# Optimization experiments

Hardware: AMD Instinct MI355X
Metric: run time of the kernel (lower is better)

## Reference

```python
import jax, jax.numpy as jnp
import numpy as np

N, D, H, O, E, K = 4096, 512, 1024, 512, 8, 2


def setup_inputs() -> dict:
    key = jax.random.key(0)
    ks = jax.random.split(key, 7)
    s = 0.02
    return {
        "x": jax.random.normal(ks[0], (N, D), dtype=jnp.float32),
        "W1": jax.random.normal(ks[1], (E, D, H), dtype=jnp.float32) * s,
        "b1": jnp.zeros((E, H), dtype=jnp.float32),
        "W2": jax.random.normal(ks[2], (E, H, O), dtype=jnp.float32) * s,
        "b2": jnp.zeros((E, O), dtype=jnp.float32),
        "Wg": jax.random.normal(ks[3], (D, E), dtype=jnp.float32) * s,
        "bg": jnp.zeros((E,), dtype=jnp.float32),
        "k": K,
    }


def reference(x, W1, b1, W2, b2, Wg, bg, k):
    # Gating: softmax over experts, then top-k with renormalized weights
    gates = jax.nn.softmax(x @ Wg + bg, axis=1)              # [N, E]
    topv, topi = jax.lax.top_k(gates, k)                     # [N, k]
    w = topv / jnp.sum(topv, axis=1, keepdims=True)          # renormalized top-k weights

    # Dense per-expert two-layer MLP (grouped GEMM form)
    h = jax.nn.relu(jnp.einsum('nd,edh->neh', x, W1) + b1[None])   # [N, E, H]
    y = jnp.einsum('neh,eho->neo', h, W2) + b2[None]               # [N, E, O]

    # Gather selected experts and combine
    y_sel = jnp.take_along_axis(y, topi[:, :, None], axis=1)       # [N, k, O]
    out = jnp.einsum('nko,nk->no', y_sel, w)                       # [N, O]
    return out, gates, topi
```

## Files before the change

### kernel.cpp

```cpp
#include <hip/hip_runtime.h>
#include <hip/hip_bf16.h>

#define N_TOK 4096
#define DIM   512
#define HID   1024
#define OUTD  512
#define NEXP  8
#define TOPK  2

#define MT1 72
#define HROWS 9216

typedef __bf16 bf16;
typedef bf16  bf16x8 __attribute__((ext_vector_type(8)));
typedef bf16  bf16x4 __attribute__((ext_vector_type(4)));
typedef float f32x4  __attribute__((ext_vector_type(4)));

__device__ inline f32x4 mfma16(bf16x8 a, bf16x8 b, f32x4 c) {
    return __builtin_amdgcn_mfma_f32_16x16x32_bf16(a, b, c, 0, 0, 0);
}

__device__ inline void gload16(const bf16* g, char* l) {
    __builtin_amdgcn_global_load_lds(
        (const __attribute__((address_space(1))) void*)g,
        (__attribute__((address_space(3))) void*)l, 16, 0, 0);
}

__global__ __launch_bounds__(256) void prep_gate_kernel(
    const float* __restrict__ W1, const float* __restrict__ W2,
    const float* __restrict__ Wg, const float* __restrict__ bg,
    const float* __restrict__ x,
    bf16* __restrict__ W1t, bf16* __restrict__ W2t,
    bf16* __restrict__ xb,
    float* __restrict__ gates_out, float* __restrict__ topi_out,
    int* __restrict__ pick_e, float* __restrict__ pick_w)
{
    __shared__ __align__(16) float smem[NEXP * DIM];
    int b = blockIdx.x;

    if (b >= 8192) {
        const float4* Wg4 = (const float4*)Wg;
        for (int i = threadIdx.x; i < DIM * NEXP / 4; i += 256) {
            float4 v = Wg4[i];
#pragma unroll
            for (int j = 0; j < 4; ++j) {
                int idx = i * 4 + j;
                smem[(idx & 7) * DIM + (idx >> 3)] = ((const float*)&v)[j];
            }
        }
        __syncthreads();

        int wave = threadIdx.x >> 6;
        int lane = threadIdx.x & 63;
        int n = (b - 8192) * 4 + wave;

        const float4* x4 = (const float4*)(x + (size_t)n * DIM);
        float4 v0 = x4[lane];
        float4 v1 = x4[lane + 64];

        bf16x4 o0 = { (bf16)v0.x, (bf16)v0.y, (bf16)v0.z, (bf16)v0.w };
        bf16x4 o1 = { (bf16)v1.x, (bf16)v1.y, (bf16)v1.z, (bf16)v1.w };
        bf16x4* xb4 = (bf16x4*)(xb + (size_t)n * DIM);
        xb4[lane]      = o0;
        xb4[lane + 64] = o1;

        float acc[NEXP];
#pragma unroll
        for (int e = 0; e < NEXP; ++e) {
            const float4* wr = (const float4*)(smem + e * DIM);
            float4 w0 = wr[lane];
            float4 w1 = wr[lane + 64];
            acc[e] = v0.x * w0.x + v0.y * w0.y + v0.z * w0.z + v0.w * w0.w
                   + v1.x * w1.x + v1.y * w1.y + v1.z * w1.z + v1.w * w1.w;
        }
#pragma unroll
        for (int off = 32; off >= 1; off >>= 1) {
#pragma unroll
            for (int e = 0; e < NEXP; ++e) acc[e] += __shfl_xor(acc[e], off, 64);
        }
#pragma unroll
        for (int e = 0; e < NEXP; ++e) acc[e] += bg[e];

        float m = acc[0];
#pragma unroll
        for (int e = 1; e < NEXP; ++e) m = fmaxf(m, acc[e]);
        float g[NEXP];
        float s = 0.f;
#pragma unroll
        for (int e = 0; e < NEXP; ++e) { g[e] = expf(acc[e] - m); s += g[e]; }
        float inv_s = 1.f / s;
#pragma unroll
        for (int e = 0; e < NEXP; ++e) g[e] *= inv_s;

        if (lane < NEXP) gates_out[n * NEXP + lane] = g[lane];

        if (lane == 0) {
            int m1 = 0;
#pragma unroll
            for (int e = 1; e < NEXP; ++e) if (g[e] > g[m1]) m1 = e;
            int m2 = (m1 == 0) ? 1 : 0;
#pragma unroll
            for (int e = 0; e < NEXP; ++e) if (e != m1 && g[e] > g[m2]) m2 = e;
            float v1g = g[m1], v2g = g[m2];
            float inv = 1.f / (v1g + v2g);
            topi_out[n * TOPK + 0] = (float)m1;
            topi_out[n * TOPK + 1] = (float)m2;
            int2 pe = { m1, m2 };
            float2 pw = { v1g * inv, v2g * inv };
            *(int2*)(pick_e + n * 2) = pe;
            *(float2*)(pick_w + n * 2) = pw;
        }
        return;
    }

    float (*tile)[33] = (float(*)[33])smem;
    const float* src; bf16* dst; int R, C, tilex, rem, e;
    if (b < 4096) {
        e = b >> 9; rem = b & 511; R = DIM; C = HID; tilex = 32;
        src = W1; dst = W1t;
    } else {
        b -= 4096;
        e = b >> 9; rem = b & 511; R = HID; C = OUTD; tilex = 16;
        src = W2; dst = W2t;
    }
    const float* s = src + (size_t)e * R * C;
    bf16* d = dst + (size_t)e * R * C;
    int c0 = (rem % tilex) * 32, r0 = (rem / tilex) * 32;

    int tx = threadIdx.x & 31, ty = threadIdx.x >> 5;
#pragma unroll
    for (int i = 0; i < 4; ++i) {
        int r = ty + i * 8;
        tile[r][tx] = s[(size_t)(r0 + r) * C + c0 + tx];
    }
    __syncthreads();

    int t = threadIdx.x;
    int dc = t >> 3, q = t & 7;
    bf16x4 v;
#pragma unroll
    for (int j = 0; j < 4; ++j) v[j] = (bf16)tile[q * 4 + j][dc];
    *(bf16x4*)(d + (size_t)(c0 + dc) * R + r0 + q * 4) = v;
}

__global__ __launch_bounds__(1024) void bucket_sched_kernel(
    const int* __restrict__ pick_e,
    int* __restrict__ counts, int* __restrict__ tlist, int* __restrict__ meta)
{
    __shared__ int cnt[NEXP];
    if (threadIdx.x < NEXP) cnt[threadIdx.x] = 0;
    __syncthreads();
    for (int i = threadIdx.x; i < N_TOK * 2; i += 1024) {
        int e = pick_e[i];
        int p = atomicAdd(&cnt[e], 1);
        tlist[e * N_TOK + p] = i;
    }
    __syncthreads();
    if (threadIdx.x == 0) {
        int base = 0, t1 = 0;
        for (int e = 0; e < NEXP; ++e) {
            int c = cnt[e];
            counts[e] = c;
            int n1 = (c + 127) >> 7;
            for (int lt = 0; lt < n1; ++lt) {
                meta[2 + t1 * 3]     = e;
                meta[2 + t1 * 3 + 1] = base + lt * 128;
                meta[2 + t1 * 3 + 2] = lt * 128;
                ++t1;
            }
            base += n1 << 7;
        }
        meta[0] = t1;
    }
}


__global__ __launch_bounds__(256, 4) void l1_kernel(
    const bf16* __restrict__ xb, const bf16* __restrict__ W1t,
    const float* __restrict__ b1, const int* __restrict__ counts,
    const int* __restrict__ tlist, const int* __restrict__ meta,
    bf16* __restrict__ h)
{
    int mt = blockIdx.x >> 3, nt = blockIdx.x & 7;
    if (mt >= meta[0]) return;
    const int* s1 = meta + 2 + mt * 3;
    int e = s1[0], rb = s1[1], i0 = s1[2];
    int cnt = counts[e];

    __shared__ __align__(16) char lds[32768];

    int tid = threadIdx.x, w = tid >> 6, l = tid & 63;
    int c0 = w * 128 + l, c1 = c0 + 64;
    int rA0 = c0 >> 2, rA1 = c1 >> 2;
    int kA0 = (c0 & 3) ^ ((rA0 & 3) ^ ((rA0 >> 2) & 1));
    int kA1 = (c1 & 3) ^ ((rA1 & 3) ^ ((rA1 >> 2) & 1));
    int iA0 = i0 + rA0, iA1 = i0 + rA1;
    int tok0 = iA0 < cnt ? (tlist[e * N_TOK + iA0] >> 1) : 0;
    int tok1 = iA1 < cnt ? (tlist[e * N_TOK + iA1] >> 1) : 0;
    const bf16* sA0 = xb + (size_t)tok0 * DIM + kA0 * 8;
    const bf16* sA1 = xb + (size_t)tok1 * DIM + kA1 * 8;
    int n0 = nt * 128;
    const bf16* w1e = W1t + (size_t)e * HID * DIM;
    const bf16* sB0 = w1e + (size_t)(n0 + rA0) * DIM + kA0 * 8;
    const bf16* sB1 = w1e + (size_t)(n0 + rA1) * DIM + kA1 * 8;
    int oA0 = c0 * 16, oA1 = c1 * 16;

    f32x4 acc[4][4];
#pragma unroll
    for (int mf = 0; mf < 4; ++mf)
#pragma unroll
        for (int nf = 0; nf < 4; ++nf) acc[mf][nf] = (f32x4){0.f, 0.f, 0.f, 0.f};

    int wm = w >> 1, wn = w & 1;
    int lr = l & 15;
    int kb = (((l >> 4) ^ ((l & 3) ^ ((l >> 2) & 1)))) * 16;

    {
        char* A = lds;       char* B = lds + 8192;
        gload16(sA0, A + oA0); gload16(sA1, A + oA1);
        gload16(sB0, B + oA0); gload16(sB1, B + oA1);
    }

    for (int ks = 0; ks < 16; ++ks) {
        __syncthreads();
        if (ks < 15) {
            char* A = lds + (((ks + 1) & 1) * 16384);
            char* B = A + 8192;
            int kof = (ks + 1) * 32;
            gload16(sA0 + kof, A + oA0); gload16(sA1 + kof, A + oA1);
            gload16(sB0 + kof, B + oA0); gload16(sB1 + kof, B + oA1);
        }
        char* A = lds + ((ks & 1) * 16384);
        char* B = A + 8192;
        bf16x8 af[4], bfr[4];
#pragma unroll
        for (int mf = 0; mf < 4; ++mf)
            af[mf] = *(const bf16x8*)(A + (wm * 64 + mf * 16 + lr) * 64 + kb);
#pragma unroll
        for (int nf = 0; nf < 4; ++nf)
            bfr[nf] = *(const bf16x8*)(B + (wn * 64 + nf * 16 + lr) * 64 + kb);
#pragma unroll
        for (int mf = 0; mf < 4; ++mf)
#pragma unroll
            for (int nf = 0; nf < 4; ++nf)
                acc[mf][nf] = mfma16(af[mf], bfr[nf], acc[mf][nf]);
    }

    const float* b1e = b1 + e * HID;
#pragma unroll
    for (int nf = 0; nf < 4; ++nf) {
        int colg = n0 + wn * 64 + nf * 16 + lr;
        float bias = b1e[colg];
#pragma unroll
        for (int mf = 0; mf < 4; ++mf) {
#pragma unroll
            for (int r = 0; r < 4; ++r) {
                int gr = rb + wm * 64 + mf * 16 + (l >> 4) * 4 + r;
                float v = fmaxf(acc[mf][nf][r] + bias, 0.f);
                h[(size_t)gr * HID + colg] = (bf16)v;
            }
        }
    }
}

__global__ __launch_bounds__(256, 4) void l2_kernel(
    const bf16* __restrict__ h, const bf16* __restrict__ W2t,
    const int* __restrict__ counts, const int* __restrict__ tlist,
    const int* __restrict__ meta, bf16* __restrict__ ybuf)
{
    int mt = blockIdx.x >> 2, nt = blockIdx.x & 3;
    if (mt >= meta[0]) return;
    const int* s1 = meta + 2 + mt * 3;
    int e = s1[0], rb = s1[1], i0 = s1[2];
    int cnt = counts[e];

    __shared__ __align__(16) char lds[32768];

    int tid = threadIdx.x, w = tid >> 6, l = tid & 63;
    int c0 = w * 128 + l, c1 = c0 + 64;
    int rA0 = c0 >> 2, rA1 = c1 >> 2;
    int kA0 = (c0 & 3) ^ ((rA0 & 3) ^ ((rA0 >> 2) & 1));
    int kA1 = (c1 & 3) ^ ((rA1 & 3) ^ ((rA1 >> 2) & 1));
    const bf16* sA0 = h + (size_t)(rb + rA0) * HID + kA0 * 8;
    const bf16* sA1 = h + (size_t)(rb + rA1) * HID + kA1 * 8;
    int n0 = nt * 128;
    const bf16* w2e = W2t + (size_t)e * OUTD * HID;
    const bf16* sB0 = w2e + (size_t)(n0 + rA0) * HID + kA0 * 8;
    const bf16* sB1 = w2e + (size_t)(n0 + rA1) * HID + kA1 * 8;
    int oA0 = c0 * 16, oA1 = c1 * 16;

    f32x4 acc[4][4];
#pragma unroll
    for (int mf = 0; mf < 4; ++mf)
#pragma unroll
        for (int nf = 0; nf < 4; ++nf) acc[mf][nf] = (f32x4){0.f, 0.f, 0.f, 0.f};

    int wm = w >> 1, wn = w & 1;
    int lr = l & 15;
    int kb = (((l >> 4) ^ ((l & 3) ^ ((l >> 2) & 1)))) * 16;

    {
        char* A = lds;       char* B = lds + 8192;
        gload16(sA0, A + oA0); gload16(sA1, A + oA1);
        gload16(sB0, B + oA0); gload16(sB1, B + oA1);
    }

    for (int ks = 0; ks < 32; ++ks) {
        __syncthreads();
        if (ks < 31) {
            char* A = lds + (((ks + 1) & 1) * 16384);
            char* B = A + 8192;
            int kof = (ks + 1) * 32;
            gload16(sA0 + kof, A + oA0); gload16(sA1 + kof, A + oA1);
            gload16(sB0 + kof, B + oA0); gload16(sB1 + kof, B + oA1);
        }
        char* A = lds + ((ks & 1) * 16384);
        char* B = A + 8192;
        bf16x8 af[4], bfr[4];
#pragma unroll
        for (int mf = 0; mf < 4; ++mf)
            af[mf] = *(const bf16x8*)(A + (wm * 64 + mf * 16 + lr) * 64 + kb);
#pragma unroll
        for (int nf = 0; nf < 4; ++nf)
            bfr[nf] = *(const bf16x8*)(B + (wn * 64 + nf * 16 + lr) * 64 + kb);
#pragma unroll
        for (int mf = 0; mf < 4; ++mf)
#pragma unroll
            for (int nf = 0; nf < 4; ++nf)
                acc[mf][nf] = mfma16(af[mf], bfr[nf], acc[mf][nf]);
    }

#pragma unroll
    for (int mf = 0; mf < 4; ++mf) {
#pragma unroll
        for (int r = 0; r < 4; ++r) {
            int rloc = wm * 64 + mf * 16 + (l >> 4) * 4 + r;
            int i = i0 + rloc;
            if (i < cnt) {
                int pi = tlist[e * N_TOK + i];
                bf16* yrow = ybuf + (size_t)pi * OUTD;
#pragma unroll
                for (int nf = 0; nf < 4; ++nf) {
                    int colg = n0 + wn * 64 + nf * 16 + lr;
                    yrow[colg] = (bf16)acc[mf][nf][r];
                }
            }
        }
    }
}

__global__ __launch_bounds__(256) void combine_kernel(
    const bf16* __restrict__ ybuf, const float* __restrict__ b2,
    const int* __restrict__ pick_e, const float* __restrict__ pick_w,
    float* __restrict__ out)
{
    int wave = threadIdx.x >> 6;
    int lane = threadIdx.x & 63;
    int n = blockIdx.x * 4 + wave;

    int e0 = pick_e[n * 2], e1 = pick_e[n * 2 + 1];
    float w0 = pick_w[n * 2], w1 = pick_w[n * 2 + 1];

    const bf16x8* y0 = (const bf16x8*)(ybuf + (size_t)(n * 2) * OUTD);
    const bf16x8* y1 = (const bf16x8*)(ybuf + (size_t)(n * 2 + 1) * OUTD);
    const float4* b20 = (const float4*)(b2 + e0 * OUTD);
    const float4* b21 = (const float4*)(b2 + e1 * OUTD);
    float4* o4 = (float4*)(out + (size_t)n * OUTD);

    bf16x8 a = y0[lane];
    bf16x8 b = y1[lane];
    float4 c0 = b20[lane * 2], c1 = b20[lane * 2 + 1];
    float4 d0 = b21[lane * 2], d1 = b21[lane * 2 + 1];

    float4 r0, r1;
    r0.x = w0 * ((float)a[0] + c0.x) + w1 * ((float)b[0] + d0.x);
    r0.y = w0 * ((float)a[1] + c0.y) + w1 * ((float)b[1] + d0.y);
    r0.z = w0 * ((float)a[2] + c0.z) + w1 * ((float)b[2] + d0.z);
    r0.w = w0 * ((float)a[3] + c0.w) + w1 * ((float)b[3] + d0.w);
    r1.x = w0 * ((float)a[4] + c1.x) + w1 * ((float)b[4] + d1.x);
    r1.y = w0 * ((float)a[5] + c1.y) + w1 * ((float)b[5] + d1.y);
    r1.z = w0 * ((float)a[6] + c1.z) + w1 * ((float)b[6] + d1.z);
    r1.w = w0 * ((float)a[7] + c1.w) + w1 * ((float)b[7] + d1.w);
    o4[lane * 2]     = r0;
    o4[lane * 2 + 1] = r1;
}

extern "C" void kernel_launch(void* const* d_in, const int* in_sizes, int n_in,
                              void* d_out, int out_size, void* d_ws, size_t ws_size,
                              hipStream_t stream)
{
    const float* x  = (const float*)d_in[0];
    const float* W1 = (const float*)d_in[1];
    const float* b1 = (const float*)d_in[2];
    const float* W2 = (const float*)d_in[3];
    const float* b2 = (const float*)d_in[4];
    const float* Wg = (const float*)d_in[5];
    const float* bg = (const float*)d_in[6];

    float* out_f   = (float*)d_out;
    float* gates_o = out_f + (size_t)N_TOK * OUTD;
    float* topi_o  = gates_o + (size_t)N_TOK * NEXP;

    char* ws = (char*)d_ws;
    size_t offW1t  = 0;
    size_t offW2t  = offW1t + (size_t)NEXP * HID * DIM * 2;
    size_t offXb   = offW2t + (size_t)NEXP * OUTD * HID * 2;
    size_t offH    = offXb + (size_t)N_TOK * DIM * 2;
    size_t offYb   = offH + (size_t)HROWS * HID * 2;
    size_t offCnt  = offYb + (size_t)N_TOK * 2 * OUTD * 2;
    size_t offTl   = offCnt + 256;
    size_t offMeta = offTl + (size_t)NEXP * N_TOK * 4;
    size_t offPkE  = offMeta + 4096;
    size_t offPkW  = offPkE + (size_t)N_TOK * 2 * 4;

    bf16*  W1t    = (bf16*)(ws + offW1t);
    bf16*  W2t    = (bf16*)(ws + offW2t);
    bf16*  xbuf   = (bf16*)(ws + offXb);
    bf16*  hbuf   = (bf16*)(ws + offH);
    bf16*  ybuf   = (bf16*)(ws + offYb);
    int*   cnts   = (int*)(ws + offCnt);
    int*   tlist  = (int*)(ws + offTl);
    int*   meta   = (int*)(ws + offMeta);
    int*   pick_e = (int*)(ws + offPkE);
    float* pick_w = (float*)(ws + offPkW);

    prep_gate_kernel<<<8192 + N_TOK / 4, 256, 0, stream>>>(
        W1, W2, Wg, bg, x, W1t, W2t, xbuf, gates_o, topi_o, pick_e, pick_w);

    bucket_sched_kernel<<<1, 1024, 0, stream>>>(pick_e, cnts, tlist, meta);

    l1_kernel<<<MT1 * 8, 256, 0, stream>>>(xbuf, W1t, b1, cnts, tlist, meta, hbuf);
    l2_kernel<<<MT1 * 4, 256, 0, stream>>>(hbuf, W2t, cnts, tlist, meta, ybuf);

    combine_kernel<<<N_TOK / 4, 256, 0, stream>>>(ybuf, b2, pick_e, pick_w, out_f);
}
```

Baseline: 76.94 us.

## Parallelize expert bucketing, derive tiles on the fly, halve L2 M-tile

Replaces the single-block bucket scheduler, which had a serial thread-0 metadata loop, with one block per expert that compacts its own token list. The GEMM kernels now compute their (expert, row base) tile mapping from the eight counts instead of reading a precomputed meta table. The L2 GEMM moves from 128x128 to 64x128 tiles, doubling its block count for better CU occupancy at the cost of less reuse of the W2 tile. The combine kernel now handles two tokens per wave and launches half as many blocks.

```diff
diff --git a/kernel.cpp b/kernel.cpp
--- a/kernel.cpp
+++ b/kernel.cpp
@@ -24,6 +24,28 @@
     __builtin_amdgcn_global_load_lds(
         (const __attribute__((address_space(1))) void*)g,
         (__attribute__((address_space(3))) void*)l, 16, 0, 0);
+}
+
+__device__ inline void find_tile(const int* cv, int mt, int& e, int& rb, int& i0, int& ce)
+{
+    int at = 0, base = 0;
+    e = 0; rb = 0; i0 = 0; ce = 0;
+#pragma unroll
+    for (int ee = 0; ee < NEXP; ++ee) {
+        int c = cv[ee]; int n1 = (c + 127) >> 7;
+        if (mt >= at && mt < at + n1) {
+            e = ee; int lt = mt - at; rb = base + lt * 128; i0 = lt * 128; ce = c;
+        }
+        at += n1; base += n1 << 7;
+    }
+}
+
+__device__ inline int tiles_total(const int* cv)
+{
+    int t = 0;
+#pragma unroll
+    for (int ee = 0; ee < NEXP; ++ee) t += (cv[ee] + 127) >> 7;
+    return t;
 }
 
 __global__ __launch_bounds__(256) void prep_gate_kernel(
@@ -143,49 +165,37 @@
     *(bf16x4*)(d + (size_t)(c0 + dc) * R + r0 + q * 4) = v;
 }
 
-__global__ __launch_bounds__(1024) void bucket_sched_kernel(
+__global__ __launch_bounds__(256) void bucket_kernel(
     const int* __restrict__ pick_e,
-    int* __restrict__ counts, int* __restrict__ tlist, int* __restrict__ meta)
-{
-    __shared__ int cnt[NEXP];
-    if (threadIdx.x < NEXP) cnt[threadIdx.x] = 0;
+    int* __restrict__ counts, int* __restrict__ tlist)
+{
+    __shared__ int cnt;
+    if (threadIdx.x == 0) cnt = 0;
     __syncthreads();
-    for (int i = threadIdx.x; i < N_TOK * 2; i += 1024) {
-        int e = pick_e[i];
-        int p = atomicAdd(&cnt[e], 1);
-        tlist[e * N_TOK + p] = i;
+    int e = blockIdx.x;
+    for (int i = threadIdx.x; i < N_TOK * 2; i += 256) {
+        if (pick_e[i] == e) {
+            int p = atomicAdd(&cnt, 1);
+            tlist[e * N_TOK + p] = i;
+        }
     }
     __syncthreads();
-    if (threadIdx.x == 0) {
-        int base = 0, t1 = 0;
-        for (int e = 0; e < NEXP; ++e) {
-            int c = cnt[e];
-            counts[e] = c;
-            int n1 = (c + 127) >> 7;
-            for (int lt = 0; lt < n1; ++lt) {
-                meta[2 + t1 * 3]     = e;
-                meta[2 + t1 * 3 + 1] = base + lt * 128;
-                meta[2 + t1 * 3 + 2] = lt * 128;
-                ++t1;
-            }
-            base += n1 << 7;
-        }
-        meta[0] = t1;
-    }
+    if (threadIdx.x == 0) counts[e] = cnt;
 }
 
 
 __global__ __launch_bounds__(256, 4) void l1_kernel(
     const bf16* __restrict__ xb, const bf16* __restrict__ W1t,
     const float* __restrict__ b1, const int* __restrict__ counts,
-    const int* __restrict__ tlist, const int* __restrict__ meta,
-    bf16* __restrict__ h)
-{
+    const int* __restrict__ tlist, bf16* __restrict__ h)
+{
+    int cv[NEXP];
+#pragma unroll
+    for (int e = 0; e < NEXP; ++e) cv[e] = counts[e];
+    if (blockIdx.x >= tiles_total(cv) * 8) return;
     int mt = blockIdx.x >> 3, nt = blockIdx.x & 7;
-    if (mt >= meta[0]) return;
-    const int* s1 = meta + 2 + mt * 3;
-    int e = s1[0], rb = s1[1], i0 = s1[2];
-    int cnt = counts[e];
+    int e, rb, i0, cnt;
+    find_tile(cv, mt, e, rb, i0, cnt);
 
     __shared__ __align__(16) char lds[32768];
 
@@ -195,8 +205,9 @@
     int kA0 = (c0 & 3) ^ ((rA0 & 3) ^ ((rA0 >> 2) & 1));
     int kA1 = (c1 & 3) ^ ((rA1 & 3) ^ ((rA1 >> 2) & 1));
     int iA0 = i0 + rA0, iA1 = i0 + rA1;
-    int tok0 = iA0 < cnt ? (tlist[e * N_TOK + iA0] >> 1) : 0;
-    int tok1 = iA1 < cnt ? (tlist[e * N_TOK + iA1] >> 1) : 0;
+    const int* tl = tlist + e * N_TOK;
+    int tok0 = iA0 < cnt ? (tl[iA0] >> 1) : 0;
+    int tok1 = iA1 < cnt ? (tl[iA1] >> 1) : 0;
     const bf16* sA0 = xb + (size_t)tok0 * DIM + kA0 * 8;
     const bf16* sA1 = xb + (size_t)tok1 * DIM + kA1 * 8;
     int n0 = nt * 128;
@@ -213,7 +224,7 @@
 
     int wm = w >> 1, wn = w & 1;
     int lr = l & 15;
-    int kb = (((l >> 4) ^ ((l & 3) ^ ((l >> 2) & 1)))) * 16;
+    int kb = ((l >> 4) ^ ((l & 3) ^ ((l >> 2) & 1))) * 16;
 
     {
         char* A = lds;       char* B = lds + 8192;
@@ -266,84 +277,87 @@
 __global__ __launch_bounds__(256, 4) void l2_kernel(
     const bf16* __restrict__ h, const bf16* __restrict__ W2t,
     const int* __restrict__ counts, const int* __restrict__ tlist,
-    const int* __restrict__ meta, bf16* __restrict__ ybuf)
-{
-    int mt = blockIdx.x >> 2, nt = blockIdx.x & 3;
-    if (mt >= meta[0]) return;
-    const int* s1 = meta + 2 + mt * 3;
-    int e = s1[0], rb = s1[1], i0 = s1[2];
-    int cnt = counts[e];
-
-    __shared__ __align__(16) char lds[32768];
+    bf16* __restrict__ ybuf)
+{
+    int cv[NEXP];
+#pragma unroll
+    for (int e = 0; e < NEXP; ++e) cv[e] = counts[e];
+    if (blockIdx.x >= tiles_total(cv) * 8) return;
+    int mth = blockIdx.x >> 2, nt = blockIdx.x & 3;
+    int mt = mth >> 1, half = mth & 1;
+    int e, rb, i0, cnt;
+    find_tile(cv, mt, e, rb, i0, cnt);
+    rb += half * 64; i0 += half * 64;
+
+    __shared__ __align__(16) char lds[24576];
 
     int tid = threadIdx.x, w = tid >> 6, l = tid & 63;
-    int c0 = w * 128 + l, c1 = c0 + 64;
-    int rA0 = c0 >> 2, rA1 = c1 >> 2;
-    int kA0 = (c0 & 3) ^ ((rA0 & 3) ^ ((rA0 >> 2) & 1));
-    int kA1 = (c1 & 3) ^ ((rA1 & 3) ^ ((rA1 >> 2) & 1));
-    const bf16* sA0 = h + (size_t)(rb + rA0) * HID + kA0 * 8;
-    const bf16* sA1 = h + (size_t)(rb + rA1) * HID + kA1 * 8;
+    int cA = tid; int rA = cA >> 2;
+    int kA = (cA & 3) ^ ((rA & 3) ^ ((rA >> 2) & 1));
+    const bf16* sA = h + (size_t)(rb + rA) * HID + kA * 8;
+    int cB0 = w * 128 + l, cB1 = cB0 + 64;
+    int rB0 = cB0 >> 2, rB1 = cB1 >> 2;
+    int kB0 = (cB0 & 3) ^ ((rB0 & 3) ^ ((rB0 >> 2) & 1));
+    int kB1 = (cB1 & 3) ^ ((rB1 & 3) ^ ((rB1 >> 2) & 1));
     int n0 = nt * 128;
     const bf16* w2e = W2t + (size_t)e * OUTD * HID;
-    const bf16* sB0 = w2e + (size_t)(n0 + rA0) * HID + kA0 * 8;
-    const bf16* sB1 = w2e + (size_t)(n0 + rA1) * HID + kA1 * 8;
-    int oA0 = c0 * 16, oA1 = c1 * 16;
-
-    f32x4 acc[4][4];
-#pragma unroll
-    for (int mf = 0; mf < 4; ++mf)
+    const bf16* sB0 = w2e + (size_t)(n0 + rB0) * HID + kB0 * 8;
+    const bf16* sB1 = w2e + (size_t)(n0 + rB1) * HID + kB1 * 8;
+    int oA = cA * 16, oB0 = cB0 * 16, oB1 = cB1 * 16;
+
+    f32x4 acc[2][4];
+#pragma unroll
+    for (int mf = 0; mf < 2; ++mf)
 #pragma unroll
         for (int nf = 0; nf < 4; ++nf) acc[mf][nf] = (f32x4){0.f, 0.f, 0.f, 0.f};
 
     int wm = w >> 1, wn = w & 1;
     int lr = l & 15;
-    int kb = (((l >> 4) ^ ((l & 3) ^ ((l >> 2) & 1)))) * 16;
+    int kb = ((l >> 4) ^ ((l & 3) ^ ((l >> 2) & 1))) * 16;
 
     {
-        char* A = lds;       char* B = lds + 8192;
-        gload16(sA0, A + oA0); gload16(sA1, A + oA1);
-        gload16(sB0, B + oA0); gload16(sB1, B + oA1);
+        char* A = lds; char* B = lds + 4096;
+        gload16(sA, A + oA); gload16(sB0, B + oB0); gload16(sB1, B + oB1);
     }
 
     for (int ks = 0; ks < 32; ++ks) {
         __syncthreads();
         if (ks < 31) {
-            char* A = lds + (((ks + 1) & 1) * 16384);
-            char* B = A + 8192;
+            char* A = lds + (((ks + 1) & 1) * 12288);
+            char* B = A + 4096;
             int kof = (ks + 1) * 32;
-            gload16(sA0 + kof, A + oA0); gload16(sA1 + kof, A + oA1);
-            gload16(sB0 + kof, B + oA0); gload16(sB1 + kof, B + oA1);
-        }
-        char* A = lds + ((ks & 1) * 16384);
-        char* B = A + 8192;
-        bf16x8 af[4], bfr[4];
-#pragma unroll
-        for (int mf = 0; mf < 4; ++mf)
-            af[mf] = *(const bf16x8*)(A + (wm * 64 + mf * 16 + lr) * 64 + kb);
+            gload16(sA + kof, A + oA);
+            gload16(sB0 + kof, B + oB0); gload16(sB1 + kof, B + oB1);
+        }
+        char* A = lds + ((ks & 1) * 12288);
+        char* B = A + 4096;
+        bf16x8 af[2], bfr[4];
+#pragma unroll
+        for (int mf = 0; mf < 2; ++mf)
+            af[mf] = *(const bf16x8*)(A + (wm * 32 + mf * 16 + lr) * 64 + kb);
 #pragma unroll
         for (int nf = 0; nf < 4; ++nf)
             bfr[nf] = *(const bf16x8*)(B + (wn * 64 + nf * 16 + lr) * 64 + kb);
 #pragma unroll
-        for (int mf = 0; mf < 4; ++mf)
+        for (int mf = 0; mf < 2; ++mf)
 #pragma unroll
             for (int nf = 0; nf < 4; ++nf)
                 acc[mf][nf] = mfma16(af[mf], bfr[nf], acc[mf][nf]);
     }
 
-#pragma unroll
-    for (int mf = 0; mf < 4; ++mf) {
+    const int* tl = tlist + e * N_TOK;
+#pragma unroll
+    for (int mf = 0; mf < 2; ++mf) {
 #pragma unroll
         for (int r = 0; r < 4; ++r) {
-            int rloc = wm * 64 + mf * 16 + (l >> 4) * 4 + r;
+            int rloc = wm * 32 + mf * 16 + (l >> 4) * 4 + r;
             int i = i0 + rloc;
             if (i < cnt) {
-                int pi = tlist[e * N_TOK + i];
+                int pi = tl[i];
                 bf16* yrow = ybuf + (size_t)pi * OUTD;
 #pragma unroll
-                for (int nf = 0; nf < 4; ++nf) {
-                    int colg = n0 + wn * 64 + nf * 16 + lr;
-                    yrow[colg] = (bf16)acc[mf][nf][r];
-                }
+                for (int nf = 0; nf < 4; ++nf)
+                    yrow[n0 + wn * 64 + nf * 16 + lr] = (bf16)acc[mf][nf][r];
             }
         }
     }
@@ -354,35 +368,37 @@
     const int* __restrict__ pick_e, const float* __restrict__ pick_w,
     float* __restrict__ out)
 {
-    int wave = threadIdx.x >> 6;
-    int lane = threadIdx.x & 63;
-    int n = blockIdx.x * 4 + wave;
-
-    int e0 = pick_e[n * 2], e1 = pick_e[n * 2 + 1];
-    float w0 = pick_w[n * 2], w1 = pick_w[n * 2 + 1];
-
-    const bf16x8* y0 = (const bf16x8*)(ybuf + (size_t)(n * 2) * OUTD);
-    const bf16x8* y1 = (const bf16x8*)(ybuf + (size_t)(n * 2 + 1) * OUTD);
-    const float4* b20 = (const float4*)(b2 + e0 * OUTD);
-    const float4* b21 = (const float4*)(b2 + e1 * OUTD);
-    float4* o4 = (float4*)(out + (size_t)n * OUTD);
-
-    bf16x8 a = y0[lane];
-    bf16x8 b = y1[lane];
-    float4 c0 = b20[lane * 2], c1 = b20[lane * 2 + 1];
-    float4 d0 = b21[lane * 2], d1 = b21[lane * 2 + 1];
-
-    float4 r0, r1;
-    r0.x = w0 * ((float)a[0] + c0.x) + w1 * ((float)b[0] + d0.x);
-    r0.y = w0 * ((float)a[1] + c0.y) + w1 * ((float)b[1] + d0.y);
-    r0.z = w0 * ((float)a[2] + c0.z) + w1 * ((float)b[2] + d0.z);
-    r0.w = w0 * ((float)a[3] + c0.w) + w1 * ((float)b[3] + d0.w);
-    r1.x = w0 * ((float)a[4] + c1.x) + w1 * ((float)b[4] + d1.x);
-    r1.y = w0 * ((float)a[5] + c1.y) + w1 * ((float)b[5] + d1.y);
-    r1.z = w0 * ((float)a[6] + c1.z) + w1 * ((float)b[6] + d1.z);
-    r1.w = w0 * ((float)a[7] + c1.w) + w1 * ((float)b[7] + d1.w);
-    o4[lane * 2]     = r0;
-    o4[lane * 2 + 1] = r1;
+    int w = threadIdx.x >> 6;
+    int l = threadIdx.x & 63;
+#pragma unroll
+    for (int j = 0; j < 2; ++j) {
+        int n = blockIdx.x * 8 + w * 2 + j;
+        int e0 = pick_e[n * 2], e1 = pick_e[n * 2 + 1];
+        float w0 = pick_w[n * 2], w1 = pick_w[n * 2 + 1];
+
+        const bf16x8* y0 = (const bf16x8*)(ybuf + (size_t)(n * 2) * OUTD);
+        const bf16x8* y1 = (const bf16x8*)(ybuf + (size_t)(n * 2 + 1) * OUTD);
+        const float4* b20 = (const float4*)(b2 + e0 * OUTD);
+        const float4* b21 = (const float4*)(b2 + e1 * OUTD);
+        float4* o4 = (float4*)(out + (size_t)n * OUTD);
+
+        bf16x8 a = y0[l];
+        bf16x8 b = y1[l];
+        float4 c0 = b20[l * 2], c1 = b20[l * 2 + 1];
+        float4 d0 = b21[l * 2], d1 = b21[l * 2 + 1];
+
+        float4 r0, r1;
+        r0.x = w0 * ((float)a[0] + c0.x) + w1 * ((float)b[0] + d0.x);
+        r0.y = w0 * ((float)a[1] + c0.y) + w1 * ((float)b[1] + d0.y);
+        r0.z = w0 * ((float)a[2] + c0.z) + w1 * ((float)b[2] + d0.z);
+        r0.w = w0 * ((float)a[3] + c0.w) + w1 * ((float)b[3] + d0.w);
+        r1.x = w0 * ((float)a[4] + c1.x) + w1 * ((float)b[4] + d1.x);
+        r1.y = w0 * ((float)a[5] + c1.y) + w1 * ((float)b[5] + d1.y);
+        r1.z = w0 * ((float)a[6] + c1.z) + w1 * ((float)b[6] + d1.z);
+        r1.w = w0 * ((float)a[7] + c1.w) + w1 * ((float)b[7] + d1.w);
+        o4[l * 2]     = r0;
+        o4[l * 2 + 1] = r1;
+    }
 }
 
 extern "C" void kernel_launch(void* const* d_in, const int* in_sizes, int n_in,
@@ -402,16 +418,15 @@
     float* topi_o  = gates_o + (size_t)N_TOK * NEXP;
 
     char* ws = (char*)d_ws;
-    size_t offW1t  = 0;
-    size_t offW2t  = offW1t + (size_t)NEXP * HID * DIM * 2;
-    size_t offXb   = offW2t + (size_t)NEXP * OUTD * HID * 2;
-    size_t offH    = offXb + (size_t)N_TOK * DIM * 2;
-    size_t offYb   = offH + (size_t)HROWS * HID * 2;
-    size_t offCnt  = offYb + (size_t)N_TOK * 2 * OUTD * 2;
-    size_t offTl   = offCnt + 256;
-    size_t offMeta = offTl + (size_t)NEXP * N_TOK * 4;
-    size_t offPkE  = offMeta + 4096;
-    size_t offPkW  = offPkE + (size_t)N_TOK * 2 * 4;
+    size_t offW1t = 0;
+    size_t offW2t = offW1t + (size_t)NEXP * HID * DIM * 2;
+    size_t offXb  = offW2t + (size_t)NEXP * OUTD * HID * 2;
+    size_t offH   = offXb + (size_t)N_TOK * DIM * 2;
+    size_t offYb  = offH + (size_t)HROWS * HID * 2;
+    size_t offCnt = offYb + (size_t)N_TOK * 2 * OUTD * 2;
+    size_t offTl  = offCnt + 256;
+    size_t offPkE = offTl + (size_t)NEXP * N_TOK * 4;
+    size_t offPkW = offPkE + (size_t)N_TOK * 2 * 4;
 
     bf16*  W1t    = (bf16*)(ws + offW1t);
     bf16*  W2t    = (bf16*)(ws + offW2t);
@@ -420,17 +435,16 @@
     bf16*  ybuf   = (bf16*)(ws + offYb);
     int*   cnts   = (int*)(ws + offCnt);
     int*   tlist  = (int*)(ws + offTl);
-    int*   meta   = (int*)(ws + offMeta);
     int*   pick_e = (int*)(ws + offPkE);
     float* pick_w = (float*)(ws + offPkW);
 
     prep_gate_kernel<<<8192 + N_TOK / 4, 256, 0, stream>>>(
         W1, W2, Wg, bg, x, W1t, W2t, xbuf, gates_o, topi_o, pick_e, pick_w);
 
-    bucket_sched_kernel<<<1, 1024, 0, stream>>>(pick_e, cnts, tlist, meta);
-
-    l1_kernel<<<MT1 * 8, 256, 0, stream>>>(xbuf, W1t, b1, cnts, tlist, meta, hbuf);
-    l2_kernel<<<MT1 * 4, 256, 0, stream>>>(hbuf, W2t, cnts, tlist, meta, ybuf);
-
-    combine_kernel<<<N_TOK / 4, 256, 0, stream>>>(ybuf, b2, pick_e, pick_w, out_f);
-}
+    bucket_kernel<<<NEXP, 256, 0, stream>>>(pick_e, cnts, tlist);
+
+    l1_kernel<<<MT1 * 8, 256, 0, stream>>>(xbuf, W1t, b1, cnts, tlist, hbuf);
+    l2_kernel<<<MT1 * 8, 256, 0, stream>>>(hbuf, W2t, cnts, tlist, ybuf);
+
+    combine_kernel<<<N_TOK / 8, 256, 0, stream>>>(ybuf, b2, pick_e, pick_w, out_f);
+}
```

Result: slower. 84.40 us (+9.7%).
